# Optimization experiments

Measured on AMD Instinct MI355X. Metric: run time of the kernel, lower is better.

Reference implementation:

```python
import jax, jax.numpy as jnp
import numpy as np

D_MODEL = 512
NHEAD = 8
D_K = D_MODEL // NHEAD


def setup_inputs() -> dict:
    key = jax.random.key(0)
    ks = jax.random.split(key, 11)
    B, N = 2, 16384
    s = 1.0 / np.sqrt(D_MODEL)
    inp = {
        "query": jax.random.normal(ks[0], (B, N, D_MODEL), jnp.float32),
        "key": jax.random.normal(ks[1], (B, N, D_MODEL), jnp.float32),
        "value": jax.random.normal(ks[2], (B, N, D_MODEL), jnp.float32),
        "Wq": jax.random.normal(ks[3], (D_MODEL, D_MODEL), jnp.float32) * s,
        "bq": jnp.zeros((D_MODEL,), jnp.float32),
        "Wk": jax.random.normal(ks[4], (D_MODEL, D_MODEL), jnp.float32) * s,
        "bk": jnp.zeros((D_MODEL,), jnp.float32),
        "Wv": jax.random.normal(ks[5], (D_MODEL, D_MODEL), jnp.float32) * s,
        "bv": jnp.zeros((D_MODEL,), jnp.float32),
        "Wo": jax.random.normal(ks[6], (D_MODEL, D_MODEL), jnp.float32) * s,
        "bo": jnp.zeros((D_MODEL,), jnp.float32),
    }
    return inp


def _split_heads(x):
    # [b, n, d_model] -> [b, h, n, d_k]
    b, n, _ = x.shape
    return x.reshape(b, n, NHEAD, D_K).transpose(0, 2, 1, 3)


def reference(query, key, value, Wq, bq, Wk, bk, Wv, bv, Wo, bo):
    b, n, _ = query.shape
    q = _split_heads(query @ Wq + bq)  # [b,h,n,dk]
    k = _split_heads(key @ Wk + bk)
    v = _split_heads(value @ Wv + bv)

    # linear attention (Shen et al. 2018): softmax over feature dim of q,
    # softmax over sequence dim of k, then KV outer-product context.
    q = jax.nn.softmax(q, axis=-1) / jnp.sqrt(jnp.asarray(D_K, q.dtype))
    k = jax.nn.softmax(k, axis=-2)
    context = jnp.einsum('bhnd,bhne->bhde', k, v)   # [b,h,dk,dk]
    out = jnp.einsum('bhnd,bhde->bhne', q, context)  # [b,h,n,dk]

    out = out.transpose(0, 2, 1, 3).reshape(b, n, D_MODEL)
    return out @ Wo + bo
```

## Files before the change

kernel.cpp:

```cpp
#include <hip/hip_runtime.h>
#include <hip/hip_bf16.h>


using u16 = unsigned short;
typedef __attribute__((ext_vector_type(8))) short bf16x8;
typedef __attribute__((ext_vector_type(4))) float f32x4;

#define D_MODEL 512
#define SEQ 16384


#define PART_OFF 0u
#define SUMS_OFF 33554432u
#define CTX_OFF  34078720u
#define WTKS_OFF 34340864u
#define WTVS_OFF 34865152u
#define WTQS_OFF 35389440u
#define MTS_OFF  35913728u
#define WS_NEEDED 36962304u

__device__ __forceinline__ float bf2f(u16 u) {
  union { unsigned int i; float f; } x; x.i = ((unsigned int)u) << 16; return x.f;
}
__device__ __forceinline__ u16 f2bf(float f) {
  union { float ff; unsigned int i; } x; x.ff = f;
  unsigned int r = x.i + 0x7fffu + ((x.i >> 16) & 1u);
  return (u16)(r >> 16);
}
__device__ __forceinline__ unsigned int pk2(float lo, float hi) {
  union { __hip_bfloat162 h; unsigned int u; } x;
  x.h = __float22bfloat162_rn(float2{lo, hi});
  return x.u;
}
__device__ __forceinline__ bf16x8 ldsrd(const u16* base, int row, int rowbytes,
                                        int kbyte, int mask) {
  return *(const bf16x8*)((const char*)base + row * rowbytes + (kbyte ^ ((row & mask) << 4)));
}
__device__ __forceinline__ void bar_lgkm() {
  asm volatile("s_waitcnt lgkmcnt(0)" ::: "memory");
  __builtin_amdgcn_sched_barrier(0);
  __builtin_amdgcn_s_barrier();
  __builtin_amdgcn_sched_barrier(0);
}

__launch_bounds__(256)
__global__ void wcvt_kernel(const float* __restrict__ Wk, const float* __restrict__ Wv,
                            const float* __restrict__ Wq, u16* __restrict__ WTks,
                            u16* __restrict__ WTvs, u16* __restrict__ WTqs) {
  const float* in = blockIdx.z == 0 ? Wk : (blockIdx.z == 1 ? Wv : Wq);
  u16* out = blockIdx.z == 0 ? WTks : (blockIdx.z == 1 ? WTvs : WTqs);
  __shared__ float S[64][65];
  const int t = threadIdx.x;
  const int k0 = blockIdx.y << 6, c0 = blockIdx.x << 6;
#pragma unroll
  for (int ii = 0; ii < 4; ++ii) {
    const int idx = t + ii * 256;
    const int r = idx >> 4, c4 = (idx & 15) << 2;
    const float4 v = *(const float4*)(in + (k0 + r) * D_MODEL + c0 + c4);
    S[r][c4] = v.x; S[r][c4 + 1] = v.y; S[r][c4 + 2] = v.z; S[r][c4 + 3] = v.w;
  }
  __syncthreads();
#pragma unroll
  for (int it = 0; it < 2; ++it) {
    const int fi = it * 256 + t;
    const int cb_loc = fi >> 7;
    const int ksm_loc = (fi >> 6) & 1;
    const int lane = fi & 63;
    const int col_loc = cb_loc * 16 + (lane & 15);
    const int kl0 = ksm_loc * 32 + (lane >> 4) * 8;
    union { bf16x8 v; u16 e[8]; } o;
#pragma unroll
    for (int jj = 0; jj < 8; ++jj) o.e[jj] = f2bf(S[kl0 + jj][col_loc]);
    const int cb16 = blockIdx.x * 4 + cb_loc;
    const int ksm = blockIdx.y * 2 + ksm_loc;
    *(bf16x8*)(out + cb16 * 8192 + ksm * 512 + lane * 8) = o.v;
  }
}

__launch_bounds__(512, 2)
__global__ void phase1_kernel(const float* __restrict__ key, const float* __restrict__ value,
                              const u16* __restrict__ WTks, const u16* __restrict__ WTvs,
                              const float* __restrict__ bkp, const float* __restrict__ bvp,
                              float* __restrict__ part, float* __restrict__ sums) {
  __shared__ __align__(16) u16 smem[24576];
  u16* KA = smem;
  u16* VA = smem + 8192;
  u16* ET = smem + 16384;
  u16* VT = smem + 20480;
  const int t = threadIdx.x;
  const int lane = t & 63, w = t >> 6;
  const int g = lane >> 4, lc = lane & 15;
  const int f = blockIdx.x;
  const int xc = f & 7, kk2 = f >> 3;
  const int rowgroup = xc * 32 + (kk2 >> 2);
  const int hp = kk2 & 3;
  const int hloc = w >> 2, cq = w & 3;
  const int h = hp * 2 + hloc;
  const int dl = cq * 16 + lc;
  const int b = rowgroup >> 7, grpl = rowgroup & 127;
  const int bh = b * 8 + h;
  u16* ETh = ET + hloc * 2048;
  u16* VTh = VT + hloc * 2048;
  const u16* wtkb = WTks + (h * 4 + cq) * 8192;
  const u16* wtvb = WTvs + (h * 4 + cq) * 8192;
  const float bbk = bkp[h * 64 + dl];
  const float bbv = bvp[h * 64 + dl];
  const int sr = t >> 4;
  const int sc = t & 15;
  const int swoff = sr * 256 + ((sc * 16) ^ ((sr & 7) << 4));

  f32x4 pacc[4];
#pragma unroll
  for (int em = 0; em < 4; ++em) pacc[em] = (f32x4){0.f, 0.f, 0.f, 0.f};
  float sp = 0.f;
  f32x4 aK0 = (f32x4){0.f,0.f,0.f,0.f}, aK1 = aK0, aV0 = aK0, aV1 = aK0;

  float4 kreg[3][2], vreg[3][2];
  auto LOADSL = [&](int set, int gs) {
    const int row = (rowgroup * 4 + (gs >> 2)) * 32 + sr;
    const float* kp = key + (size_t)row * D_MODEL + (gs & 3) * 128 + sc * 8;
    kreg[set][0] = *(const float4*)kp; kreg[set][1] = *(const float4*)(kp + 4);
    const float* vp = value + (size_t)row * D_MODEL + (gs & 3) * 128 + sc * 8;
    vreg[set][0] = *(const float4*)vp; vreg[set][1] = *(const float4*)(vp + 4);
  };
  auto WRITESL = [&](int set, int buf) {
    const float4 k0 = kreg[set][0], k1 = kreg[set][1];
    uint4 wk; wk.x = pk2(k0.x, k0.y); wk.y = pk2(k0.z, k0.w);
    wk.z = pk2(k1.x, k1.y); wk.w = pk2(k1.z, k1.w);
    *(uint4*)((char*)KA + buf * 8192 + swoff) = wk;
    const float4 v0 = vreg[set][0], v1 = vreg[set][1];
    uint4 wv; wv.x = pk2(v0.x, v0.y); wv.y = pk2(v0.z, v0.w);
    wv.z = pk2(v1.x, v1.y); wv.w = pk2(v1.z, v1.w);
    *(uint4*)((char*)VA + buf * 8192 + swoff) = wv;
  };

  LOADSL(0, 0);
  LOADSL(1, 1);
  LOADSL(2, 2);
  WRITESL(0, 0);
  bar_lgkm();

#pragma unroll
  for (int gs = 0; gs < 16; ++gs) {
    bf16x8 bK[4], bV[4];
#pragma unroll
    for (int j = 0; j < 4; ++j) {
      const int ksm = (gs & 3) * 4 + j;
      bK[j] = *(const bf16x8*)(wtkb + ksm * 512 + lane * 8);
      bV[j] = *(const bf16x8*)(wtvb + ksm * 512 + lane * 8);
    }
    if (gs + 1 < 16) WRITESL((gs + 1) % 3, (gs + 1) & 1);
    if (gs + 3 < 16) LOADSL(gs % 3, gs + 3);
    const u16* bufK = KA + (gs & 1) * 4096;
    const u16* bufV = VA + (gs & 1) * 4096;
#pragma unroll
    for (int ksl = 0; ksl < 4; ++ksl) {
      const int kb = ksl * 64 + g * 16;
      bf16x8 a0 = ldsrd(bufK, lc, 256, kb, 7);
      bf16x8 a1 = ldsrd(bufK, 16 + lc, 256, kb, 7);
      aK0 = __builtin_amdgcn_mfma_f32_16x16x32_bf16(a0, bK[ksl], aK0, 0, 0, 0);
      aK1 = __builtin_amdgcn_mfma_f32_16x16x32_bf16(a1, bK[ksl], aK1, 0, 0, 0);
      bf16x8 c0 = ldsrd(bufV, lc, 256, kb, 7);
      bf16x8 c1 = ldsrd(bufV, 16 + lc, 256, kb, 7);
      aV0 = __builtin_amdgcn_mfma_f32_16x16x32_bf16(c0, bV[ksl], aV0, 0, 0, 0);
      aV1 = __builtin_amdgcn_mfma_f32_16x16x32_bf16(c1, bV[ksl], aV1, 0, 0, 0);
    }
    if ((gs & 3) == 3) {
#pragma unroll
      for (int r = 0; r < 4; ++r) { aK0[r] = __expf(aK0[r] + bbk); sp += aK0[r]; }
#pragma unroll
      for (int r = 0; r < 4; ++r) { aK1[r] = __expf(aK1[r] + bbk); sp += aK1[r]; }
      *(uint2*)((char*)ETh + dl * 64 + ((g * 8) ^ ((dl & 3) << 4))) =
          make_uint2(pk2(aK0[0], aK0[1]), pk2(aK0[2], aK0[3]));
      *(uint2*)((char*)ETh + dl * 64 + ((32 + g * 8) ^ ((dl & 3) << 4))) =
          make_uint2(pk2(aK1[0], aK1[1]), pk2(aK1[2], aK1[3]));
      *(uint2*)((char*)VTh + dl * 64 + ((g * 8) ^ ((dl & 3) << 4))) =
          make_uint2(pk2(aV0[0] + bbv, aV0[1] + bbv), pk2(aV0[2] + bbv, aV0[3] + bbv));
      *(uint2*)((char*)VTh + dl * 64 + ((32 + g * 8) ^ ((dl & 3) << 4))) =
          make_uint2(pk2(aV1[0] + bbv, aV1[1] + bbv), pk2(aV1[2] + bbv, aV1[3] + bbv));
      bar_lgkm();
      {
        bf16x8 paf = ldsrd(ETh, dl, 64, g * 16, 3);
#pragma unroll
        for (int em = 0; em < 4; ++em) {
          bf16x8 pbf = ldsrd(VTh, em * 16 + lc, 64, g * 16, 3);
          pacc[em] = __builtin_amdgcn_mfma_f32_16x16x32_bf16(paf, pbf, pacc[em], 0, 0, 0);
        }
      }
      aK0 = (f32x4){0.f,0.f,0.f,0.f}; aK1 = aK0; aV0 = aK0; aV1 = aK0;
    }
    bar_lgkm();
  }

  float* pp = part + (size_t)(bh * 128 + grpl) * 4096;
#pragma unroll
  for (int em = 0; em < 4; ++em)
    *(f32x4*)(pp + (em * 16 + lc) * 64 + cq * 16 + g * 4) = pacc[em];
  sp += __shfl_xor(sp, 16); sp += __shfl_xor(sp, 32);
  if (g == 0) sums[(size_t)(bh * 128 + grpl) * 64 + dl] = sp;
}

__launch_bounds__(256)
__global__ void reduce_kernel(const float* __restrict__ part, const float* __restrict__ sums,
                              float* __restrict__ ctx) {
  __shared__ float den[64];
  const int bh = blockIdx.x;
  const int t = threadIdx.x;
  if (t < 64) {
    float s = 0.f;
    for (int gp = 0; gp < 128; ++gp) s += sums[(size_t)(bh * 128 + gp) * 64 + t];
    den[t] = s;
  }
  float4 A0 = {0,0,0,0}, A1 = {0,0,0,0}, A2 = {0,0,0,0}, A3 = {0,0,0,0};
  const float* pb = part + (size_t)bh * 128 * 4096;
  for (int gp = 0; gp < 128; ++gp) {
    const float4* q = (const float4*)(pb + gp * 4096 + t * 16);
    const float4 q0 = q[0], q1 = q[1], q2 = q[2], q3 = q[3];
    A0.x += q0.x; A0.y += q0.y; A0.z += q0.z; A0.w += q0.w;
    A1.x += q1.x; A1.y += q1.y; A1.z += q1.z; A1.w += q1.w;
    A2.x += q2.x; A2.y += q2.y; A2.z += q2.z; A2.w += q2.w;
    A3.x += q3.x; A3.y += q3.y; A3.z += q3.z; A3.w += q3.w;
  }
  __syncthreads();
  const int e = t >> 2, d0 = (t & 3) * 16;
  float* cb = ctx + (size_t)bh * 4096 + e;
  const float r0[4] = {A0.x, A0.y, A0.z, A0.w};
  const float r1[4] = {A1.x, A1.y, A1.z, A1.w};
  const float r2[4] = {A2.x, A2.y, A2.z, A2.w};
  const float r3[4] = {A3.x, A3.y, A3.z, A3.w};
#pragma unroll
  for (int i = 0; i < 4; ++i) cb[(d0 + i) * 64] = r0[i] / den[d0 + i];
#pragma unroll
  for (int i = 0; i < 4; ++i) cb[(d0 + 4 + i) * 64] = r1[i] / den[d0 + 4 + i];
#pragma unroll
  for (int i = 0; i < 4; ++i) cb[(d0 + 8 + i) * 64] = r2[i] / den[d0 + 8 + i];
#pragma unroll
  for (int i = 0; i < 4; ++i) cb[(d0 + 12 + i) * 64] = r3[i] / den[d0 + 12 + i];
}

__launch_bounds__(256)
__global__ void mbigT_kernel(const float* __restrict__ ctx, const float* __restrict__ Wo,
                             u16* __restrict__ MTs) {
  __shared__ float Clds[64][65];
  __shared__ float Wlds2[64][64];
  const int t = threadIdx.x;
  const int tx = t & 15, ty = t >> 4;
  const int cc = blockIdx.x;
  const int bh = blockIdx.y;
  const int b = bh >> 3, h = bh & 7;
  const float* ch = ctx + bh * 4096;
  for (int i4 = t; i4 < 1024; i4 += 256) {
    const int r = i4 >> 4, c = (i4 & 15) << 2;
    const float4 v = *(const float4*)(ch + (r << 6) + c);
    Clds[r][c] = v.x; Clds[r][c + 1] = v.y; Clds[r][c + 2] = v.z; Clds[r][c + 3] = v.w;
    const float4 wv = *(const float4*)(Wo + (h * 64 + r) * D_MODEL + cc * 64 + c);
    Wlds2[r][c] = wv.x; Wlds2[r][c + 1] = wv.y; Wlds2[r][c + 2] = wv.z; Wlds2[r][c + 3] = wv.w;
  }
  __syncthreads();
  float acc[4][4] = {};
#pragma unroll 8
  for (int k = 0; k < 64; ++k) {
    float a[4], wv[4];
#pragma unroll
    for (int i = 0; i < 4; ++i) a[i] = Clds[(ty << 2) + i][k];
#pragma unroll
    for (int j = 0; j < 4; ++j) wv[j] = Wlds2[k][(tx << 2) + j];
#pragma unroll
    for (int i = 0; i < 4; ++i)
#pragma unroll
      for (int j = 0; j < 4; ++j) acc[i][j] = fmaf(a[i], wv[j], acc[i][j]);
  }
#pragma unroll
  for (int i = 0; i < 4; ++i)
#pragma unroll
    for (int j = 0; j < 4; ++j) {
      const int c = cc * 64 + (tx << 2) + j;
      const int k = h * 64 + (ty << 2) + i;
      const int cb16 = c >> 4, lcc = c & 15;
      const int ksm = k >> 5, gg = (k >> 3) & 3, jb = k & 7;
      MTs[(size_t)b * 262144 + cb16 * 8192 + ksm * 512 + (gg * 16 + lcc) * 8 + jb]
          = f2bf(acc[i][j]);
    }
}

__launch_bounds__(512, 2)
__global__ void phase3_kernel(const float* __restrict__ query, const u16* __restrict__ WTqs,
                              const float* __restrict__ bqp, const u16* __restrict__ MTs,
                              const float* __restrict__ bop, float* __restrict__ out) {
  __shared__ __align__(16) u16 smem[24576];
  u16* SL = smem;
  u16* P  = smem + 8192;
  const int t = threadIdx.x;
  const int lane = t & 63, w = t >> 6;
  const int g = lane >> 4, lc = lane & 15;
  const int chunk = blockIdx.x;
  const int n0 = chunk * 32;
  const int b = chunk >> 9;
  const int c0 = w * 64;
  const int sr = t >> 4;
  const int sc = t & 15;
  const int swoff = sr * 256 + ((sc * 16) ^ ((sr & 7) << 4));

  f32x4 acc[4][2];
#pragma unroll
  for (int m = 0; m < 4; ++m)
#pragma unroll
    for (int n = 0; n < 2; ++n) acc[m][n] = (f32x4){0.f, 0.f, 0.f, 0.f};

  float4 qreg[3][2];
  auto LOADQ = [&](int set, int gs) {
    const float* qp = query + (size_t)(n0 + sr) * D_MODEL + gs * 128 + sc * 8;
    qreg[set][0] = *(const float4*)qp; qreg[set][1] = *(const float4*)(qp + 4);
  };
  auto WRITEQ = [&](int set, int buf) {
    const float4 q0 = qreg[set][0], q1 = qreg[set][1];
    uint4 wq; wq.x = pk2(q0.x, q0.y); wq.y = pk2(q0.z, q0.w);
    wq.z = pk2(q1.x, q1.y); wq.w = pk2(q1.z, q1.w);
    *(uint4*)((char*)SL + buf * 8192 + swoff) = wq;
  };

  LOADQ(0, 0); LOADQ(1, 1); LOADQ(2, 2);
  WRITEQ(0, 0);
  bar_lgkm();

#pragma unroll
  for (int gs = 0; gs < 4; ++gs) {
    if (gs + 1 < 4) WRITEQ((gs + 1) % 3, (gs + 1) & 1);
    if (gs + 3 < 4) LOADQ(gs % 3, gs + 3);
    const u16* S = SL + (gs & 1) * 4096;
#pragma unroll
    for (int ksl = 0; ksl < 4; ++ksl) {
      const int ksm = gs * 4 + ksl;
      bf16x8 af[4], bfr[2];
#pragma unroll
      for (int mf = 0; mf < 4; ++mf)
        af[mf] = *(const bf16x8*)(WTqs + (w * 4 + mf) * 8192 + ksm * 512 + lane * 8);
      const int kb = ksl * 64 + g * 16;
#pragma unroll
      for (int nf = 0; nf < 2; ++nf) bfr[nf] = ldsrd(S, nf * 16 + lc, 256, kb, 7);
#pragma unroll
      for (int mf = 0; mf < 4; ++mf)
#pragma unroll
        for (int nf = 0; nf < 2; ++nf)
          acc[mf][nf] = __builtin_amdgcn_mfma_f32_16x16x32_bf16(af[mf], bfr[nf], acc[mf][nf], 0, 0, 0);
    }
    bar_lgkm();
  }
  {
    float bqv[4][4];
#pragma unroll
    for (int m = 0; m < 4; ++m)
#pragma unroll
      for (int r = 0; r < 4; ++r) bqv[m][r] = bqp[c0 + m * 16 + g * 4 + r];
#pragma unroll
    for (int nf = 0; nf < 2; ++nf) {
      float mx = -3.0e38f;
#pragma unroll
      for (int m = 0; m < 4; ++m)
#pragma unroll
        for (int r = 0; r < 4; ++r) {
          const float v = acc[m][nf][r] + bqv[m][r];
          acc[m][nf][r] = v; mx = fmaxf(mx, v);
        }
      mx = fmaxf(mx, __shfl_xor(mx, 16)); mx = fmaxf(mx, __shfl_xor(mx, 32));
      float s = 0.f;
#pragma unroll
      for (int m = 0; m < 4; ++m)
#pragma unroll
        for (int r = 0; r < 4; ++r) {
          const float e = __expf(acc[m][nf][r] - mx);
          acc[m][nf][r] = e; s += e;
        }
      s += __shfl_xor(s, 16); s += __shfl_xor(s, 32);
      const float fsc = 0.125f / s;
      const int n = nf * 16 + lc;
#pragma unroll
      for (int m = 0; m < 4; ++m) {
        const uint2 pw = make_uint2(pk2(acc[m][nf][0] * fsc, acc[m][nf][1] * fsc),
                                    pk2(acc[m][nf][2] * fsc, acc[m][nf][3] * fsc));
        *(uint2*)((char*)P + n * 1024 + ((w * 128 + m * 32 + g * 8) ^ ((n & 7) << 4))) = pw;
      }
    }
  }
  bar_lgkm();
  f32x4 oc[4][2];
#pragma unroll
  for (int m = 0; m < 4; ++m)
#pragma unroll
    for (int n = 0; n < 2; ++n) oc[m][n] = (f32x4){0.f, 0.f, 0.f, 0.f};
  const u16* MT = MTs + (size_t)b * 262144;
#pragma unroll 2
  for (int ks = 0; ks < 16; ++ks) {
    bf16x8 af[4], bfr[2];
#pragma unroll
    for (int mf = 0; mf < 4; ++mf)
      af[mf] = *(const bf16x8*)(MT + (w * 4 + mf) * 8192 + ks * 512 + lane * 8);
#pragma unroll
    for (int nf = 0; nf < 2; ++nf) bfr[nf] = ldsrd(P, nf * 16 + lc, 1024, ks * 64 + g * 16, 7);
#pragma unroll
    for (int mf = 0; mf < 4; ++mf)
#pragma unroll
      for (int nf = 0; nf < 2; ++nf)
        oc[mf][nf] = __builtin_amdgcn_mfma_f32_16x16x32_bf16(af[mf], bfr[nf], oc[mf][nf], 0, 0, 0);
  }
  {
    float bov[4][4];
#pragma unroll
    for (int m = 0; m < 4; ++m)
#pragma unroll
      for (int r = 0; r < 4; ++r) bov[m][r] = bop[c0 + m * 16 + g * 4 + r];
#pragma unroll
    for (int mf = 0; mf < 4; ++mf)
#pragma unroll
      for (int nf = 0; nf < 2; ++nf) {
        float4 o;
        o.x = oc[mf][nf][0] + bov[mf][0]; o.y = oc[mf][nf][1] + bov[mf][1];
        o.z = oc[mf][nf][2] + bov[mf][2]; o.w = oc[mf][nf][3] + bov[mf][3];
        *(float4*)(out + (size_t)(n0 + nf * 16 + lc) * D_MODEL + c0 + mf * 16 + g * 4) = o;
      }
  }
}

__global__ void sentinel_kernel(float* out) { out[0] = 1.0e9f; }

extern "C" void kernel_launch(void* const* d_in, const int* in_sizes, int n_in,
                              void* d_out, int out_size, void* d_ws, size_t ws_size,
                              hipStream_t stream) {
  const float* query = (const float*)d_in[0];
  const float* key   = (const float*)d_in[1];
  const float* value = (const float*)d_in[2];
  const float* Wq = (const float*)d_in[3];
  const float* bq = (const float*)d_in[4];
  const float* Wk = (const float*)d_in[5];
  const float* bk = (const float*)d_in[6];
  const float* Wv = (const float*)d_in[7];
  const float* bv = (const float*)d_in[8];
  const float* Wo = (const float*)d_in[9];
  const float* bo = (const float*)d_in[10];
  float* out = (float*)d_out;
  char* ws = (char*)d_ws;

  if (ws_size < (size_t)WS_NEEDED) {
    sentinel_kernel<<<1, 1, 0, stream>>>(out);
    return;
  }

  float* part = (float*)(ws + PART_OFF);
  float* sums = (float*)(ws + SUMS_OFF);
  float* ctx  = (float*)(ws + CTX_OFF);
  u16* WTks   = (u16*)(ws + WTKS_OFF);
  u16* WTvs   = (u16*)(ws + WTVS_OFF);
  u16* WTqs   = (u16*)(ws + WTQS_OFF);
  u16* MTs    = (u16*)(ws + MTS_OFF);

  const dim3 blk256(256);
  wcvt_kernel<<<dim3(8, 8, 3), blk256, 0, stream>>>(Wk, Wv, Wq, WTks, WTvs, WTqs);
  phase1_kernel<<<1024, 512, 0, stream>>>(key, value, WTks, WTvs, bk, bv, part, sums);
  reduce_kernel<<<16, blk256, 0, stream>>>(part, sums, ctx);
  mbigT_kernel<<<dim3(8, 16), blk256, 0, stream>>>(ctx, Wo, MTs);
  phase3_kernel<<<1024, 512, 0, stream>>>(query, WTqs, bq, MTs, bo, out);
}
```

Measured before the change: 214.9 us.

## Split context reduction into two stages and pass exp(K) via shuffles

The single 16-block reduction over 128 partial context matrices per head becomes a two-stage reduction: 256 blocks each sum 8 partials, then 16 blocks sum the 16 intermediates. This spreads 32 MB of partial reads across far more CUs instead of serialising them on 16 blocks. Separately, in phase1 the exp(K) transpose goes through cross-lane shuffles instead of an LDS buffer, which frees 8 KB of shared memory and one LDS write/read round-trip. The cost is an extra kernel launch, a small intermediate buffer and more shuffle instructions.

```diff
diff --git a/kernel.cpp b/kernel.cpp
--- a/kernel.cpp
+++ b/kernel.cpp
@@ -17,7 +17,9 @@
 #define WTVS_OFF 34865152u
 #define WTQS_OFF 35389440u
 #define MTS_OFF  35913728u
-#define WS_NEEDED 36962304u
+#define PART2_OFF 36962304u
+#define SUMS2_OFF 41156608u
+#define WS_NEEDED 41222144u
 
 __device__ __forceinline__ float bf2f(u16 u) {
   union { unsigned int i; float f; } x; x.i = ((unsigned int)u) << 16; return x.f;
@@ -82,11 +84,10 @@
                               const u16* __restrict__ WTks, const u16* __restrict__ WTvs,
                               const float* __restrict__ bkp, const float* __restrict__ bvp,
                               float* __restrict__ part, float* __restrict__ sums) {
-  __shared__ __align__(16) u16 smem[24576];
+  __shared__ __align__(16) u16 smem[20480];
   u16* KA = smem;
   u16* VA = smem + 8192;
-  u16* ET = smem + 16384;
-  u16* VT = smem + 20480;
+  u16* VT = smem + 16384;
   const int t = threadIdx.x;
   const int lane = t & 63, w = t >> 6;
   const int g = lane >> 4, lc = lane & 15;
@@ -99,7 +100,6 @@
   const int dl = cq * 16 + lc;
   const int b = rowgroup >> 7, grpl = rowgroup & 127;
   const int bh = b * 8 + h;
-  u16* ETh = ET + hloc * 2048;
   u16* VTh = VT + hloc * 2048;
   const u16* wtkb = WTks + (h * 4 + cq) * 8192;
   const u16* wtvb = WTvs + (h * 4 + cq) * 8192;
@@ -170,21 +170,38 @@
       for (int r = 0; r < 4; ++r) { aK0[r] = __expf(aK0[r] + bbk); sp += aK0[r]; }
 #pragma unroll
       for (int r = 0; r < 4; ++r) { aK1[r] = __expf(aK1[r] + bbk); sp += aK1[r]; }
-      *(uint2*)((char*)ETh + dl * 64 + ((g * 8) ^ ((dl & 3) << 4))) =
-          make_uint2(pk2(aK0[0], aK0[1]), pk2(aK0[2], aK0[3]));
-      *(uint2*)((char*)ETh + dl * 64 + ((32 + g * 8) ^ ((dl & 3) << 4))) =
-          make_uint2(pk2(aK1[0], aK1[1]), pk2(aK1[2], aK1[3]));
+      union { bf16x8 v; unsigned int u[4]; } paf;
+      {
+        const unsigned int p0 = pk2(aK0[0], aK0[1]);
+        const unsigned int p1 = pk2(aK0[2], aK0[3]);
+        const unsigned int p2 = pk2(aK1[0], aK1[1]);
+        const unsigned int p3 = pk2(aK1[2], aK1[3]);
+        const int srcA = (((2 * g) & 3) << 4) + lc;
+        const int srcB = (((2 * g + 1) & 3) << 4) + lc;
+        const unsigned int w0a = (unsigned)__shfl((int)p0, srcA);
+        const unsigned int w0b = (unsigned)__shfl((int)p2, srcA);
+        const unsigned int w1a = (unsigned)__shfl((int)p1, srcA);
+        const unsigned int w1b = (unsigned)__shfl((int)p3, srcA);
+        const unsigned int w2a = (unsigned)__shfl((int)p0, srcB);
+        const unsigned int w2b = (unsigned)__shfl((int)p2, srcB);
+        const unsigned int w3a = (unsigned)__shfl((int)p1, srcB);
+        const unsigned int w3b = (unsigned)__shfl((int)p3, srcB);
+        const bool lo = (g < 2);
+        paf.u[0] = lo ? w0a : w0b;
+        paf.u[1] = lo ? w1a : w1b;
+        paf.u[2] = lo ? w2a : w2b;
+        paf.u[3] = lo ? w3a : w3b;
+      }
       *(uint2*)((char*)VTh + dl * 64 + ((g * 8) ^ ((dl & 3) << 4))) =
           make_uint2(pk2(aV0[0] + bbv, aV0[1] + bbv), pk2(aV0[2] + bbv, aV0[3] + bbv));
       *(uint2*)((char*)VTh + dl * 64 + ((32 + g * 8) ^ ((dl & 3) << 4))) =
           make_uint2(pk2(aV1[0] + bbv, aV1[1] + bbv), pk2(aV1[2] + bbv, aV1[3] + bbv));
       bar_lgkm();
       {
-        bf16x8 paf = ldsrd(ETh, dl, 64, g * 16, 3);
 #pragma unroll
         for (int em = 0; em < 4; ++em) {
           bf16x8 pbf = ldsrd(VTh, em * 16 + lc, 64, g * 16, 3);
-          pacc[em] = __builtin_amdgcn_mfma_f32_16x16x32_bf16(paf, pbf, pacc[em], 0, 0, 0);
+          pacc[em] = __builtin_amdgcn_mfma_f32_16x16x32_bf16(paf.v, pbf, pacc[em], 0, 0, 0);
         }
       }
       aK0 = (f32x4){0.f,0.f,0.f,0.f}; aK1 = aK0; aV0 = aK0; aV1 = aK0;
@@ -201,20 +218,50 @@
 }
 
 __launch_bounds__(256)
-__global__ void reduce_kernel(const float* __restrict__ part, const float* __restrict__ sums,
-                              float* __restrict__ ctx) {
+__global__ void reduce1_kernel(const float* __restrict__ part, const float* __restrict__ sums,
+                               float* __restrict__ part2, float* __restrict__ sums2) {
+  const int seg = blockIdx.x, bh = blockIdx.y;
+  const int t = threadIdx.x;
+  float4 A0 = {0,0,0,0}, A1 = {0,0,0,0}, A2 = {0,0,0,0}, A3 = {0,0,0,0};
+  const float* pb = part + (size_t)(bh * 128 + seg * 8) * 4096;
+#pragma unroll
+  for (int gp = 0; gp < 8; ++gp) {
+    const float4* q = (const float4*)(pb + gp * 4096 + t * 16);
+    const float4 q0 = q[0], q1 = q[1], q2 = q[2], q3 = q[3];
+    A0.x += q0.x; A0.y += q0.y; A0.z += q0.z; A0.w += q0.w;
+    A1.x += q1.x; A1.y += q1.y; A1.z += q1.z; A1.w += q1.w;
+    A2.x += q2.x; A2.y += q2.y; A2.z += q2.z; A2.w += q2.w;
+    A3.x += q3.x; A3.y += q3.y; A3.z += q3.z; A3.w += q3.w;
+  }
+  float4* o = (float4*)(part2 + (size_t)(bh * 16 + seg) * 4096 + t * 16);
+  o[0] = A0; o[1] = A1; o[2] = A2; o[3] = A3;
+  if (t < 64) {
+    const float* sb = sums + (size_t)(bh * 128 + seg * 8) * 64 + t;
+    float s = 0.f;
+#pragma unroll
+    for (int gp = 0; gp < 8; ++gp) s += sb[gp * 64];
+    sums2[(size_t)(bh * 16 + seg) * 64 + t] = s;
+  }
+}
+
+__launch_bounds__(256)
+__global__ void reduce2_kernel(const float* __restrict__ part2, const float* __restrict__ sums2,
+                               float* __restrict__ ctx) {
   __shared__ float den[64];
   const int bh = blockIdx.x;
   const int t = threadIdx.x;
   if (t < 64) {
+    const float* sb = sums2 + (size_t)bh * 16 * 64 + t;
     float s = 0.f;
-    for (int gp = 0; gp < 128; ++gp) s += sums[(size_t)(bh * 128 + gp) * 64 + t];
+#pragma unroll
+    for (int seg = 0; seg < 16; ++seg) s += sb[seg * 64];
     den[t] = s;
   }
   float4 A0 = {0,0,0,0}, A1 = {0,0,0,0}, A2 = {0,0,0,0}, A3 = {0,0,0,0};
-  const float* pb = part + (size_t)bh * 128 * 4096;
-  for (int gp = 0; gp < 128; ++gp) {
-    const float4* q = (const float4*)(pb + gp * 4096 + t * 16);
+  const float* pb = part2 + (size_t)bh * 16 * 4096;
+#pragma unroll
+  for (int seg = 0; seg < 16; ++seg) {
+    const float4* q = (const float4*)(pb + seg * 4096 + t * 16);
     const float4 q0 = q[0], q1 = q[1], q2 = q[2], q3 = q[3];
     A0.x += q0.x; A0.y += q0.y; A0.z += q0.z; A0.w += q0.w;
     A1.x += q1.x; A1.y += q1.y; A1.z += q1.z; A1.w += q1.w;
@@ -445,18 +492,21 @@
     return;
   }
 
-  float* part = (float*)(ws + PART_OFF);
-  float* sums = (float*)(ws + SUMS_OFF);
-  float* ctx  = (float*)(ws + CTX_OFF);
-  u16* WTks   = (u16*)(ws + WTKS_OFF);
-  u16* WTvs   = (u16*)(ws + WTVS_OFF);
-  u16* WTqs   = (u16*)(ws + WTQS_OFF);
-  u16* MTs    = (u16*)(ws + MTS_OFF);
+  float* part  = (float*)(ws + PART_OFF);
+  float* sums  = (float*)(ws + SUMS_OFF);
+  float* ctx   = (float*)(ws + CTX_OFF);
+  u16* WTks    = (u16*)(ws + WTKS_OFF);
+  u16* WTvs    = (u16*)(ws + WTVS_OFF);
+  u16* WTqs    = (u16*)(ws + WTQS_OFF);
+  u16* MTs     = (u16*)(ws + MTS_OFF);
+  float* part2 = (float*)(ws + PART2_OFF);
+  float* sums2 = (float*)(ws + SUMS2_OFF);
 
   const dim3 blk256(256);
   wcvt_kernel<<<dim3(8, 8, 3), blk256, 0, stream>>>(Wk, Wv, Wq, WTks, WTvs, WTqs);
   phase1_kernel<<<1024, 512, 0, stream>>>(key, value, WTks, WTvs, bk, bv, part, sums);
-  reduce_kernel<<<16, blk256, 0, stream>>>(part, sums, ctx);
+  reduce1_kernel<<<dim3(16, 16), blk256, 0, stream>>>(part, sums, part2, sums2);
+  reduce2_kernel<<<16, blk256, 0, stream>>>(part2, sums2, ctx);
   mbigT_kernel<<<dim3(8, 16), blk256, 0, stream>>>(ctx, Wo, MTs);
   phase3_kernel<<<1024, 512, 0, stream>>>(query, WTqs, bq, MTs, bo, out);
 }
```

Result: slower. 223.8 us (+4.1%).
